# Kernel optimization log

Measured on AMD Instinct MI355X. Metric: run time of the kernel, lower is better.

The kernel has to match this reference:

```python
import jax, jax.numpy as jnp
import numpy as np

N_STRUCT = 1000   # number of structures (segments for energy reduction)
N_SPECIES = 4


def _species_mlp(x, z, W1, b1, W2, b2, W3, b3, Wskip, bskip):
    """Species-dispatched MLP with linear skip: per-atom scalar energy [N, 1].

    For each species s, atoms with z == s go through a 2-hidden-layer tanh MLP
    plus a linear skip connection from the input features. Species count is a
    small fixed constant, so a Python loop over species with where-masking is
    the jit-friendly vectorized form of torch's masked dispatch.
    """
    out = jnp.zeros((x.shape[0], 1), dtype=x.dtype)
    for s in range(W1.shape[0]):
        h = jnp.tanh(x @ W1[s] + b1[s])
        h = jnp.tanh(h @ W2[s] + b2[s])
        y = h @ W3[s] + b3[s] + x @ Wskip[s] + bskip[s]
        out = jnp.where((z == s)[:, None], y, out)
    return out


def setup_inputs() -> dict:
    key = jax.random.key(0)
    ks = jax.random.split(key, 10)
    N, F, H, P, S = 100000, 256, 256, 200000, N_SPECIES
    ps_tensor = jax.random.normal(ks[0], (N, F), dtype=jnp.float32)
    ps_z = jax.random.randint(ks[1], (N,), 0, S)
    structure_map = jnp.sort(jax.random.randint(ks[2], (N,), 0, N_STRUCT))
    ps_tensor_grad = jax.random.normal(ks[3], (P, 3, F), dtype=jnp.float32)
    gradient_map = jax.random.randint(ks[4], (P,), 0, N)
    W1 = jax.random.normal(ks[5], (S, F, H), dtype=jnp.float32) * (F ** -0.5)
    b1 = jnp.zeros((S, H), dtype=jnp.float32)
    W2 = jax.random.normal(ks[6], (S, H, H), dtype=jnp.float32) * (H ** -0.5)
    b2 = jnp.zeros((S, H), dtype=jnp.float32)
    W3 = jax.random.normal(ks[7], (S, H, 1), dtype=jnp.float32) * (H ** -0.5)
    b3 = jnp.zeros((S, 1), dtype=jnp.float32)
    Wskip = jax.random.normal(ks[8], (S, F, 1), dtype=jnp.float32) * (F ** -0.5)
    bskip = jnp.zeros((S, 1), dtype=jnp.float32)
    return dict(ps_tensor=ps_tensor, ps_z=ps_z, structure_map=structure_map,
                ps_tensor_grad=ps_tensor_grad, gradient_map=gradient_map,
                W1=W1, b1=b1, W2=W2, b2=b2, W3=W3, b3=b3,
                Wskip=Wskip, bskip=bskip)


def reference(ps_tensor, ps_z, structure_map, ps_tensor_grad, gradient_map,
              W1, b1, W2, b2, W3, b3, Wskip, bskip):
    # per-atom energies and their input-gradient (torch.autograd.grad equivalent)
    per_atom_fn = lambda x: _species_mlp(x, ps_z, W1, b1, W2, b2, W3, b3, Wskip, bskip)
    nn_per_atom, vjp_fn = jax.vjp(per_atom_fn, ps_tensor)   # [N, 1]

    # energies: index_add_ atoms -> structures
    energies = jax.ops.segment_sum(nn_per_atom, structure_map, num_segments=N_STRUCT)  # [N_STRUCT, 1]

    # dE/d ps_tensor, since energies is a plain sum over atoms per structure
    (nn_grads,) = vjp_fn(jnp.ones_like(nn_per_atom))        # [N, F]

    # forces: gather grad per pair, contract over features, scatter-add to atoms
    per_pair = -jnp.sum(ps_tensor_grad * nn_grads[gradient_map][:, None, :], axis=-1)  # [P, 3]
    forces = jax.ops.segment_sum(per_pair, gradient_map, num_segments=ps_tensor.shape[0])  # [N, 3]
    return energies, forces
```

## Files before the change

kernel.cpp:

```cpp
#include <hip/hip_runtime.h>
#include <cstddef>

#define F 256
#define H 256
#define NSTRUCT 1000
#define NSPEC 4
#define TM 64
#define TPAD 264

typedef __attribute__((ext_vector_type(8))) short bf16x8;
typedef __attribute__((ext_vector_type(4))) float f32x4;

__device__ __forceinline__ unsigned short f2bf(float v) {
  unsigned int u = __float_as_uint(v);
  unsigned int r = (u + 0x7FFFu + ((u >> 16) & 1u)) >> 16;
  return (unsigned short)r;
}

__device__ __forceinline__ float bf2f(unsigned short v) {
  return __uint_as_float(((unsigned int)v) << 16);
}

__device__ __forceinline__ float tanh_fast(float x) {
  x = fminf(fmaxf(x, -15.f), 15.f);
  float e = __expf(2.f * x);
  return __fdividef(e - 1.f, e + 1.f);
}


__global__ void prep_w(const float* __restrict__ W1, const float* __restrict__ W2,
                       unsigned short* __restrict__ Out) {
  int t = blockIdx.x * 256 + threadIdx.x;
  if (t >= 4 * NSPEC * 8192) return;
  int m = t >> 15;
  int u = t & 32767;
  int lane = u & 63, jt = (u >> 6) & 15, kk = (u >> 10) & 7, s = u >> 13;
  int trans = (m >= 2);
  const float* In = (m == 0 || m == 3) ? W1 : W2;
  int j = jt * 16 + (lane & 15);
  int k0 = kk * 32 + (lane >> 4) * 8;
  const float* base = In + (size_t)s * F * H;
  unsigned short o[8];
  #pragma unroll
  for (int i = 0; i < 8; ++i) {
    int k = k0 + i;
    float v = trans ? base[(size_t)j * 256 + k] : base[(size_t)k * 256 + j];
    o[i] = f2bf(v);
  }
  *(ushort4*)(Out + (size_t)t * 8) = make_ushort4(o[0], o[1], o[2], o[3]);
  *(ushort4*)(Out + (size_t)t * 8 + 4) = make_ushort4(o[4], o[5], o[6], o[7]);
}

__global__ void histogram_kernel(const int* __restrict__ z, int* __restrict__ cnt, int N) {
  int i = blockIdx.x * blockDim.x + threadIdx.x;
  int lane = threadIdx.x & 63;
  int zi = (i < N) ? z[i] : -1;
  #pragma unroll
  for (int s = 0; s < NSPEC; ++s) {
    unsigned long long m = __ballot(zi == s);
    if (m != 0ull && lane == __ffsll((unsigned long long)m) - 1)
      atomicAdd(&cnt[s], __popcll(m));
  }
}

__global__ void scan_kernel(int* __restrict__ cnt, int* __restrict__ poff) {
  int acc = 0;
  for (int s = 0; s < NSPEC; ++s) {
    poff[s] = acc;
    int padded = ((cnt[s] + TM - 1) / TM) * TM;
    acc += padded;
    cnt[s] = 0;
  }
  poff[NSPEC] = acc;
}

__global__ void scatter_kernel(const int* __restrict__ z, const int* __restrict__ poff,
                               int* __restrict__ cnt, int* __restrict__ perm, int N) {
  int i = blockIdx.x * blockDim.x + threadIdx.x;
  int lane = threadIdx.x & 63;
  int zi = (i < N) ? z[i] : -1;
  #pragma unroll
  for (int s = 0; s < NSPEC; ++s) {
    unsigned long long m = __ballot(zi == s);
    if (m == 0ull) continue;
    int leader = __ffsll((unsigned long long)m) - 1;
    int base = 0;
    if (lane == leader) base = atomicAdd(&cnt[s], __popcll(m));
    base = __shfl(base, leader, 64);
    if (zi == s) {
      int rank = __popcll(m & ((1ull << lane) - 1ull));
      perm[poff[s] + base + rank] = i;
    }
  }
}


__device__ __forceinline__ void gemm64(const unsigned short (*src)[TPAD],
                                       const unsigned short* __restrict__ wf,
                                       int w, int lane, f32x4 acc[4][2]) {
  const int l15 = lane & 15, lk = lane >> 4;
  #pragma unroll
  for (int rt = 0; rt < 4; ++rt)
    #pragma unroll
    for (int q = 0; q < 2; ++q) acc[rt][q] = (f32x4){0.f, 0.f, 0.f, 0.f};
  #pragma unroll
  for (int kk = 0; kk < 8; ++kk) {
    const int kcol = kk * 32 + lk * 8;
    bf16x8 a0 = *(const bf16x8*)&src[l15][kcol];
    bf16x8 a1 = *(const bf16x8*)&src[16 + l15][kcol];
    bf16x8 a2 = *(const bf16x8*)&src[32 + l15][kcol];
    bf16x8 a3 = *(const bf16x8*)&src[48 + l15][kcol];
    #pragma unroll
    for (int q = 0; q < 2; ++q) {
      const int jt = w * 2 + q;
      bf16x8 b = *(const bf16x8*)(wf + ((size_t)(kk * 16 + jt) * 64 + lane) * 8);
      acc[0][q] = __builtin_amdgcn_mfma_f32_16x16x32_bf16(a0, b, acc[0][q], 0, 0, 0);
      acc[1][q] = __builtin_amdgcn_mfma_f32_16x16x32_bf16(a1, b, acc[1][q], 0, 0, 0);
      acc[2][q] = __builtin_amdgcn_mfma_f32_16x16x32_bf16(a2, b, acc[2][q], 0, 0, 0);
      acc[3][q] = __builtin_amdgcn_mfma_f32_16x16x32_bf16(a3, b, acc[3][q], 0, 0, 0);
    }
  }
}


__global__ __launch_bounds__(512, 4) void mlp_fused(
    const float* __restrict__ X, const int* __restrict__ smap,
    const unsigned short* __restrict__ Wf,
    const float* __restrict__ b1g, const float* __restrict__ b2g,
    const float* __restrict__ W3g, const float* __restrict__ b3g,
    const float* __restrict__ Wskipg, const float* __restrict__ bskipg,
    const int* __restrict__ perm, const int* __restrict__ poff,
    float* __restrict__ energies, unsigned short* __restrict__ nng)
{
  __shared__ __align__(16) unsigned short bufA[TM][TPAD];
  __shared__ __align__(16) unsigned short bufB[TM][TPAD];
  __shared__ float xskp[TM][8];
  __shared__ float e_lds[TM];
  __shared__ int atom_l[TM];

  const int tid = threadIdx.x;
  const int row0 = blockIdx.x * TM;
  if (row0 >= poff[NSPEC]) return;

  int s = 0;
  #pragma unroll
  for (int q = 1; q < NSPEC; ++q)
    if (row0 >= poff[q]) s = q;

  const size_t WMAT = (size_t)NSPEC * 65536;
  const unsigned short* w1f  = Wf + (size_t)s * 65536;
  const unsigned short* w2f  = Wf + WMAT + (size_t)s * 65536;
  const unsigned short* w2tf = Wf + 2 * WMAT + (size_t)s * 65536;
  const unsigned short* w1tf = Wf + 3 * WMAT + (size_t)s * 65536;
  const float* wsk = Wskipg + s * F;

  {
    const int lr = tid >> 3, lc = tid & 7;
    if (tid < TM) { e_lds[tid] = 0.f; atom_l[tid] = perm[row0 + tid]; }
    const int atomR = perm[row0 + lr];
    float xsk = 0.f;
    if (atomR >= 0) {
      const f32x4* xrow = (const f32x4*)(X + (size_t)atomR * F);
      #pragma unroll
      for (int jj = 0; jj < 8; ++jj) {
        const int fi = lc + jj * 8;
        f32x4 v = __builtin_nontemporal_load(xrow + fi);
        float4 wv = ((const float4*)wsk)[fi];
        xsk += v[0] * wv.x + v[1] * wv.y + v[2] * wv.z + v[3] * wv.w;
        *(ushort4*)&bufA[lr][fi * 4] =
            make_ushort4(f2bf(v[0]), f2bf(v[1]), f2bf(v[2]), f2bf(v[3]));
      }
    } else {
      #pragma unroll
      for (int jj = 0; jj < 8; ++jj)
        *(ushort4*)&bufA[lr][(lc + jj * 8) * 4] = make_ushort4(0, 0, 0, 0);
    }
    xskp[lr][lc] = xsk;
  }
  __syncthreads();

  const int w = tid >> 6, lane = tid & 63;
  const int l15 = lane & 15, lk = lane >> 4;
  f32x4 acc[4][2];

  gemm64(bufA, w1f, w, lane, acc);
  #pragma unroll
  for (int q = 0; q < 2; ++q) {
    const int col = (w * 2 + q) * 16 + l15;
    const float b1v = b1g[s * H + col];
    #pragma unroll
    for (int rt = 0; rt < 4; ++rt) {
      const int rowb = rt * 16 + lk * 4;
      #pragma unroll
      for (int r = 0; r < 4; ++r)
        bufB[rowb + r][col] = f2bf(tanh_fast(acc[rt][q][r] + b1v));
    }
  }
  __syncthreads();

  gemm64(bufB, w2f, w, lane, acc);
  {
    float ep[4][4];
    #pragma unroll
    for (int rt = 0; rt < 4; ++rt)
      #pragma unroll
      for (int r = 0; r < 4; ++r) ep[rt][r] = 0.f;
    #pragma unroll
    for (int q = 0; q < 2; ++q) {
      const int col = (w * 2 + q) * 16 + l15;
      const float b2v = b2g[s * H + col];
      const float w3v = W3g[s * H + col];
      #pragma unroll
      for (int rt = 0; rt < 4; ++rt) {
        const int rowb = rt * 16 + lk * 4;
        #pragma unroll
        for (int r = 0; r < 4; ++r) {
          float h = tanh_fast(acc[rt][q][r] + b2v);
          ep[rt][r] += h * w3v;
          bufA[rowb + r][col] = f2bf((1.f - h * h) * w3v);
        }
      }
    }
    #pragma unroll
    for (int rt = 0; rt < 4; ++rt)
      #pragma unroll
      for (int r = 0; r < 4; ++r) {
        #pragma unroll
        for (int m = 1; m <= 8; m <<= 1)
          ep[rt][r] += __shfl_xor(ep[rt][r], m, 64);
      }
    if (l15 == 0) {
      #pragma unroll
      for (int rt = 0; rt < 4; ++rt)
        #pragma unroll
        for (int r = 0; r < 4; ++r)
          atomicAdd(&e_lds[rt * 16 + lk * 4 + r], ep[rt][r]);
    }
  }
  __syncthreads();

  if (tid < TM) {
    int atom = atom_l[tid];
    if (atom >= 0) {
      float xs = 0.f;
      #pragma unroll
      for (int q = 0; q < 8; ++q) xs += xskp[tid][q];
      atomicAdd(&energies[smap[atom]], e_lds[tid] + xs + b3g[s] + bskipg[s]);
    }
  }

  gemm64(bufA, w2tf, w, lane, acc);
  #pragma unroll
  for (int q = 0; q < 2; ++q) {
    const int col = (w * 2 + q) * 16 + l15;
    #pragma unroll
    for (int rt = 0; rt < 4; ++rt) {
      const int rowb = rt * 16 + lk * 4;
      #pragma unroll
      for (int r = 0; r < 4; ++r) {
        float h = bf2f(bufB[rowb + r][col]);
        bufB[rowb + r][col] = f2bf((1.f - h * h) * acc[rt][q][r]);
      }
    }
  }
  __syncthreads();

  gemm64(bufB, w1tf, w, lane, acc);
  #pragma unroll
  for (int q = 0; q < 2; ++q) {
    const int col = (w * 2 + q) * 16 + l15;
    const float wv = wsk[col];
    #pragma unroll
    for (int rt = 0; rt < 4; ++rt) {
      #pragma unroll
      for (int r = 0; r < 4; ++r) {
        int atom2 = atom_l[rt * 16 + lk * 4 + r];
        if (atom2 >= 0)
          nng[(size_t)atom2 * F + col] = f2bf(acc[rt][q][r] + wv);
      }
    }
  }
}


__global__ __launch_bounds__(256) void force_kernel(
    const float* __restrict__ ptg, const int* __restrict__ gmap,
    const unsigned short* __restrict__ g, float* __restrict__ forces, int P)
{
  int w = (int)((blockIdx.x * 256 + threadIdx.x) >> 6);
  int lane = threadIdx.x & 63;
  if (w >= P) return;
  int a = gmap[w];
  ushort4 gu = *(const ushort4*)(g + (size_t)a * F + lane * 4);
  float g0 = bf2f(gu.x), g1 = bf2f(gu.y), g2 = bf2f(gu.z), g3 = bf2f(gu.w);
  const f32x4* gr = (const f32x4*)(ptg + (size_t)w * 3 * F);
  f32x4 t0 = __builtin_nontemporal_load(gr + 0 * 64 + lane);
  f32x4 t1 = __builtin_nontemporal_load(gr + 1 * 64 + lane);
  f32x4 t2 = __builtin_nontemporal_load(gr + 2 * 64 + lane);
  float s0 = t0[0] * g0 + t0[1] * g1 + t0[2] * g2 + t0[3] * g3;
  float s1 = t1[0] * g0 + t1[1] * g1 + t1[2] * g2 + t1[3] * g3;
  float s2 = t2[0] * g0 + t2[1] * g1 + t2[2] * g2 + t2[3] * g3;
  #pragma unroll
  for (int off = 32; off >= 1; off >>= 1) {
    s0 += __shfl_xor(s0, off, 64);
    s1 += __shfl_xor(s1, off, 64);
    s2 += __shfl_xor(s2, off, 64);
  }
  float r = (lane == 0) ? s0 : ((lane == 1) ? s1 : s2);
  if (lane < 3) atomicAdd(&forces[(size_t)a * 3 + lane], -r);
}


extern "C" void kernel_launch(void* const* d_in, const int* in_sizes, int n_in,
                              void* d_out, int out_size, void* d_ws, size_t ws_size,
                              hipStream_t stream) {
  const float* X     = (const float*)d_in[0];
  const int*   z     = (const int*)d_in[1];
  const int*   smap  = (const int*)d_in[2];
  const float* ptg   = (const float*)d_in[3];
  const int*   gmap  = (const int*)d_in[4];
  const float* W1    = (const float*)d_in[5];
  const float* b1    = (const float*)d_in[6];
  const float* W2    = (const float*)d_in[7];
  const float* b2    = (const float*)d_in[8];
  const float* W3    = (const float*)d_in[9];
  const float* b3    = (const float*)d_in[10];
  const float* Wskip = (const float*)d_in[11];
  const float* bskip = (const float*)d_in[12];

  const int N = in_sizes[1];
  const int P = in_sizes[4];

  char* ws = (char*)d_ws;
  int* cnt  = (int*)ws;
  int* poff = (int*)(ws + 16);
  int* perm = (int*)(ws + 64);
  size_t perm_bytes = (size_t)(N + NSPEC * TM) * sizeof(int);
  size_t off = 64 + perm_bytes;
  off = (off + 255) & ~(size_t)255;
  unsigned short* Wf = (unsigned short*)(ws + off);
  const size_t WMAT = (size_t)NSPEC * 65536;
  off += 4 * WMAT * sizeof(unsigned short);
  off = (off + 255) & ~(size_t)255;
  unsigned short* nng = (unsigned short*)(ws + off);

  float* energies = (float*)d_out;
  float* forces   = energies + NSTRUCT;

  hipMemsetAsync(d_out, 0, (size_t)out_size * sizeof(float), stream);
  hipMemsetAsync(cnt, 0, 16, stream);
  hipMemsetAsync(perm, 0xFF, perm_bytes, stream);

  prep_w<<<(4 * NSPEC * 8192 + 255) / 256, 256, 0, stream>>>(W1, W2, Wf);

  histogram_kernel<<<(N + 255) / 256, 256, 0, stream>>>(z, cnt, N);
  scan_kernel<<<1, 1, 0, stream>>>(cnt, poff);
  scatter_kernel<<<(N + 255) / 256, 256, 0, stream>>>(z, poff, cnt, perm, N);

  int mlpBlocks = (N + NSPEC * TM + TM - 1) / TM;
  mlp_fused<<<mlpBlocks, 512, 0, stream>>>(X, smap, Wf, b1, b2, W3, b3,
                                           Wskip, bskip, perm, poff,
                                           energies, nng);

  int forceBlocks = (int)(((size_t)P * 64 + 255) / 256);
  force_kernel<<<forceBlocks, 256, 0, stream>>>(ptg, gmap, nng, forces, P);
}
```

Measured before the change: 399.1 us.

## Fuse force contraction into MLP kernel via per-tile pair bucketing

Pairs are bucketed by the MLP tile that owns their target atom, using an inverse permutation, a histogram, a scan and a scatter pass. The MLP kernel then keeps the input gradient in LDS and computes the per-pair force contractions directly. This removes the global write and gather of the bf16 gradient array and the separate force kernel launch. In exchange it adds three preprocessing kernels over the pairs and risks load imbalance, since each tile's pair count varies and the large streaming read of ptg now runs inside the heavy MLP blocks.

```diff
diff --git a/kernel.cpp b/kernel.cpp
--- a/kernel.cpp
+++ b/kernel.cpp
@@ -75,7 +75,8 @@
 }
 
 __global__ void scatter_kernel(const int* __restrict__ z, const int* __restrict__ poff,
-                               int* __restrict__ cnt, int* __restrict__ perm, int N) {
+                               int* __restrict__ cnt, int* __restrict__ perm,
+                               int* __restrict__ inv, int N) {
   int i = blockIdx.x * blockDim.x + threadIdx.x;
   int lane = threadIdx.x & 63;
   int zi = (i < N) ? z[i] : -1;
@@ -89,9 +90,61 @@
     base = __shfl(base, leader, 64);
     if (zi == s) {
       int rank = __popcll(m & ((1ull << lane) - 1ull));
-      perm[poff[s] + base + rank] = i;
-    }
-  }
+      int pos = poff[s] + base + rank;
+      perm[pos] = i;
+      inv[i] = pos;
+    }
+  }
+}
+
+
+__global__ void pair_hist(const int* __restrict__ gmap, const int* __restrict__ inv,
+                          int* __restrict__ phist, int P) {
+  int p = blockIdx.x * 256 + threadIdx.x;
+  if (p >= P) return;
+  atomicAdd(&phist[inv[gmap[p]] >> 6], 1);
+}
+
+__global__ void pair_scan(const int* __restrict__ phist, int* __restrict__ pbase, int nb) {
+  __shared__ int tsum[512];
+  const int tid = threadIdx.x;
+  int v[4];
+  int s = 0;
+  #pragma unroll
+  for (int j = 0; j < 4; ++j) {
+    int idx = tid * 4 + j;
+    v[j] = (idx < nb) ? phist[idx] : 0;
+    s += v[j];
+  }
+  tsum[tid] = s;
+  __syncthreads();
+  for (int off = 1; off < 512; off <<= 1) {
+    int a = tsum[tid];
+    int b = (tid >= off) ? tsum[tid - off] : 0;
+    __syncthreads();
+    tsum[tid] = a + b;
+    __syncthreads();
+  }
+  int excl = (tid == 0) ? 0 : tsum[tid - 1];
+  #pragma unroll
+  for (int j = 0; j < 4; ++j) {
+    int idx = tid * 4 + j;
+    if (idx <= nb) pbase[idx] = excl;
+    excl += v[j];
+  }
+}
+
+__global__ void pair_scatter(const int* __restrict__ gmap, const int* __restrict__ inv,
+                             const int* __restrict__ pbase, int* __restrict__ pcur,
+                             int* __restrict__ sp_pair, int* __restrict__ sp_meta, int P) {
+  int p = blockIdx.x * 256 + threadIdx.x;
+  if (p >= P) return;
+  int a = gmap[p];
+  int slot = inv[a];
+  int t = slot >> 6;
+  int pos = pbase[t] + atomicAdd(&pcur[t], 1);
+  sp_pair[pos] = p;
+  sp_meta[pos] = (a << 6) | (slot & 63);
 }
 
 
@@ -130,7 +183,10 @@
     const float* __restrict__ W3g, const float* __restrict__ b3g,
     const float* __restrict__ Wskipg, const float* __restrict__ bskipg,
     const int* __restrict__ perm, const int* __restrict__ poff,
-    float* __restrict__ energies, unsigned short* __restrict__ nng)
+    float* __restrict__ energies,
+    const float* __restrict__ ptg,
+    const int* __restrict__ sp_pair, const int* __restrict__ sp_meta,
+    const int* __restrict__ pbase, float* __restrict__ forces)
 {
   __shared__ __align__(16) unsigned short bufA[TM][TPAD];
   __shared__ __align__(16) unsigned short bufB[TM][TPAD];
@@ -272,42 +328,41 @@
     const float wv = wsk[col];
     #pragma unroll
     for (int rt = 0; rt < 4; ++rt) {
-      #pragma unroll
-      for (int r = 0; r < 4; ++r) {
-        int atom2 = atom_l[rt * 16 + lk * 4 + r];
-        if (atom2 >= 0)
-          nng[(size_t)atom2 * F + col] = f2bf(acc[rt][q][r] + wv);
+      const int rowb = rt * 16 + lk * 4;
+      #pragma unroll
+      for (int r = 0; r < 4; ++r)
+        bufA[rowb + r][col] = f2bf(acc[rt][q][r] + wv);
+    }
+  }
+  __syncthreads();
+
+  {
+    const int pb0 = pbase[blockIdx.x];
+    const int pb1 = pbase[blockIdx.x + 1];
+    for (int i = pb0 + w; i < pb1; i += 8) {
+      const int p = sp_pair[i];
+      const int meta = sp_meta[i];
+      const int sl = meta & 63;
+      const int a = meta >> 6;
+      ushort4 gu = *(const ushort4*)&bufA[sl][lane * 4];
+      float g0 = bf2f(gu.x), g1 = bf2f(gu.y), g2 = bf2f(gu.z), g3 = bf2f(gu.w);
+      const f32x4* gr = (const f32x4*)(ptg + (size_t)p * 3 * F);
+      f32x4 t0 = __builtin_nontemporal_load(gr + 0 * 64 + lane);
+      f32x4 t1 = __builtin_nontemporal_load(gr + 1 * 64 + lane);
+      f32x4 t2 = __builtin_nontemporal_load(gr + 2 * 64 + lane);
+      float s0 = t0[0] * g0 + t0[1] * g1 + t0[2] * g2 + t0[3] * g3;
+      float s1 = t1[0] * g0 + t1[1] * g1 + t1[2] * g2 + t1[3] * g3;
+      float s2 = t2[0] * g0 + t2[1] * g1 + t2[2] * g2 + t2[3] * g3;
+      #pragma unroll
+      for (int off = 32; off >= 1; off >>= 1) {
+        s0 += __shfl_xor(s0, off, 64);
+        s1 += __shfl_xor(s1, off, 64);
+        s2 += __shfl_xor(s2, off, 64);
       }
-    }
-  }
-}
-
-
-__global__ __launch_bounds__(256) void force_kernel(
-    const float* __restrict__ ptg, const int* __restrict__ gmap,
-    const unsigned short* __restrict__ g, float* __restrict__ forces, int P)
-{
-  int w = (int)((blockIdx.x * 256 + threadIdx.x) >> 6);
-  int lane = threadIdx.x & 63;
-  if (w >= P) return;
-  int a = gmap[w];
-  ushort4 gu = *(const ushort4*)(g + (size_t)a * F + lane * 4);
-  float g0 = bf2f(gu.x), g1 = bf2f(gu.y), g2 = bf2f(gu.z), g3 = bf2f(gu.w);
-  const f32x4* gr = (const f32x4*)(ptg + (size_t)w * 3 * F);
-  f32x4 t0 = __builtin_nontemporal_load(gr + 0 * 64 + lane);
-  f32x4 t1 = __builtin_nontemporal_load(gr + 1 * 64 + lane);
-  f32x4 t2 = __builtin_nontemporal_load(gr + 2 * 64 + lane);
-  float s0 = t0[0] * g0 + t0[1] * g1 + t0[2] * g2 + t0[3] * g3;
-  float s1 = t1[0] * g0 + t1[1] * g1 + t1[2] * g2 + t1[3] * g3;
-  float s2 = t2[0] * g0 + t2[1] * g1 + t2[2] * g2 + t2[3] * g3;
-  #pragma unroll
-  for (int off = 32; off >= 1; off >>= 1) {
-    s0 += __shfl_xor(s0, off, 64);
-    s1 += __shfl_xor(s1, off, 64);
-    s2 += __shfl_xor(s2, off, 64);
-  }
-  float r = (lane == 0) ? s0 : ((lane == 1) ? s1 : s2);
-  if (lane < 3) atomicAdd(&forces[(size_t)a * 3 + lane], -r);
+      float rr = (lane == 0) ? s0 : ((lane == 1) ? s1 : s2);
+      if (lane < 3) atomicAdd(&forces[(size_t)a * 3 + lane], -rr);
+    }
+  }
 }
 
 
@@ -330,38 +385,51 @@
 
   const int N = in_sizes[1];
   const int P = in_sizes[4];
+  const int nb = (N + NSPEC * TM + TM - 1) / TM;
 
   char* ws = (char*)d_ws;
-  int* cnt  = (int*)ws;
-  int* poff = (int*)(ws + 16);
-  int* perm = (int*)(ws + 64);
-  size_t perm_bytes = (size_t)(N + NSPEC * TM) * sizeof(int);
-  size_t off = 64 + perm_bytes;
+  size_t off = 0;
+  int* cnt  = (int*)(ws + off); off += 16;
+  int* poff = (int*)(ws + off); off += 48;
+  int* perm = (int*)(ws + off); off += (size_t)(N + NSPEC * TM) * sizeof(int);
+  off = (off + 255) & ~(size_t)255;
+  int* inv = (int*)(ws + off); off += (size_t)N * sizeof(int);
   off = (off + 255) & ~(size_t)255;
   unsigned short* Wf = (unsigned short*)(ws + off);
   const size_t WMAT = (size_t)NSPEC * 65536;
   off += 4 * WMAT * sizeof(unsigned short);
   off = (off + 255) & ~(size_t)255;
-  unsigned short* nng = (unsigned short*)(ws + off);
+  int* phist = (int*)(ws + off); off += (size_t)nb * sizeof(int);
+  off = (off + 255) & ~(size_t)255;
+  int* pcur = (int*)(ws + off); off += (size_t)nb * sizeof(int);
+  off = (off + 255) & ~(size_t)255;
+  int* pbase = (int*)(ws + off); off += (size_t)(nb + 1) * sizeof(int);
+  off = (off + 255) & ~(size_t)255;
+  int* sp_pair = (int*)(ws + off); off += (size_t)P * sizeof(int);
+  off = (off + 255) & ~(size_t)255;
+  int* sp_meta = (int*)(ws + off); off += (size_t)P * sizeof(int);
 
   float* energies = (float*)d_out;
   float* forces   = energies + NSTRUCT;
 
   hipMemsetAsync(d_out, 0, (size_t)out_size * sizeof(float), stream);
   hipMemsetAsync(cnt, 0, 16, stream);
-  hipMemsetAsync(perm, 0xFF, perm_bytes, stream);
+  hipMemsetAsync(perm, 0xFF, (size_t)(N + NSPEC * TM) * sizeof(int), stream);
+  hipMemsetAsync(phist, 0, (size_t)nb * sizeof(int), stream);
+  hipMemsetAsync(pcur, 0, (size_t)nb * sizeof(int), stream);
 
   prep_w<<<(4 * NSPEC * 8192 + 255) / 256, 256, 0, stream>>>(W1, W2, Wf);
 
   histogram_kernel<<<(N + 255) / 256, 256, 0, stream>>>(z, cnt, N);
   scan_kernel<<<1, 1, 0, stream>>>(cnt, poff);
-  scatter_kernel<<<(N + 255) / 256, 256, 0, stream>>>(z, poff, cnt, perm, N);
-
-  int mlpBlocks = (N + NSPEC * TM + TM - 1) / TM;
-  mlp_fused<<<mlpBlocks, 512, 0, stream>>>(X, smap, Wf, b1, b2, W3, b3,
-                                           Wskip, bskip, perm, poff,
-                                           energies, nng);
-
-  int forceBlocks = (int)(((size_t)P * 64 + 255) / 256);
-  force_kernel<<<forceBlocks, 256, 0, stream>>>(ptg, gmap, nng, forces, P);
-}
+  scatter_kernel<<<(N + 255) / 256, 256, 0, stream>>>(z, poff, cnt, perm, inv, N);
+
+  pair_hist<<<(P + 255) / 256, 256, 0, stream>>>(gmap, inv, phist, P);
+  pair_scan<<<1, 512, 0, stream>>>(phist, pbase, nb);
+  pair_scatter<<<(P + 255) / 256, 256, 0, stream>>>(gmap, inv, pbase, pcur,
+                                                    sp_pair, sp_meta, P);
+
+  mlp_fused<<<nb, 512, 0, stream>>>(X, smap, Wf, b1, b2, W3, b3,
+                                    Wskip, bskip, perm, poff, energies,
+                                    ptg, sp_pair, sp_meta, pbase, forces);
+}
```

Result: slower. 488.9 us (+22.5%).
